# Kernel optimization log

Hardware: AMD Instinct MI355X
Metric: run time of the kernel (lower is better)

Reference implementation:

```python
import jax, jax.numpy as jnp
import numpy as np

B, T, D, U = 128, 1024, 256, 256


def setup_inputs() -> dict:
    key = jax.random.key(0)
    ks = jax.random.split(key, 16)
    s_in = 1.0 / np.sqrt(D)
    s_rec = 1.0 / np.sqrt(U)
    inp = {"x": jax.random.normal(ks[0], (B, T, D), dtype=jnp.float32)}
    for i, name in enumerate(["wf", "wi", "wc", "wo"]):
        inp[name] = jax.random.normal(ks[1 + i], (D, U), dtype=jnp.float32) * s_in
    for i, name in enumerate(["rf", "ri", "rc", "ro", "pf", "pi", "po"]):
        inp[name] = jax.random.normal(ks[5 + i], (U, U), dtype=jnp.float32) * s_rec
    for i, name in enumerate(["bf", "bi", "bc", "bo"]):
        inp[name] = jax.random.normal(ks[12 + i], (U,), dtype=jnp.float32) * 0.01
    return inp


def reference(x, wf, wi, wc, wo, rf, ri, rc, ro, pf, pi, po, bf, bi, bc, bo):
    # Peephole LSTM: scan over time, state (c, h) each [B, U].
    def step(carry, xt):
        c, h = carry
        f_gate = jax.nn.sigmoid(xt @ wf + h @ rf + c @ pf + bf)
        i_gate = jax.nn.sigmoid(xt @ wi + h @ ri + c @ pi + bi)
        c_tild = jnp.tanh(xt @ wc + h @ rc + bc)
        c_new = f_gate * c + i_gate * c_tild
        o_gate = jax.nn.sigmoid(xt @ wo + h @ ro + c_new @ po + bo)
        h_new = jnp.tanh(c_new) * o_gate
        return (c_new, h_new), None

    b = x.shape[0]
    u = wf.shape[1]
    c0 = jnp.zeros((b, u), dtype=x.dtype)
    h0 = jnp.zeros((b, u), dtype=x.dtype)
    (_, h_final), _ = jax.lax.scan(step, (c0, h0), jnp.swapaxes(x, 0, 1))  # time-major [T,B,D]
    return h_final
```

## Files before the change

### kernel.cpp

```cpp
#include <hip/hip_runtime.h>

#define TT 1024
#define DU 256

#define CEX_OFF   0
#define HEX_OFF   65536
#define STMP_OFF  131072
#define TST_OFF   139264
#define GCON_OFF  172032
#define BLOB_OFF  174080
#define CHUNK_ELEMS (11*16*256)

typedef unsigned short ushort_t;
typedef unsigned u32;
typedef unsigned long long u64;
typedef __attribute__((ext_vector_type(8))) short short8;
typedef __attribute__((ext_vector_type(2))) unsigned long long u64x2;
typedef __attribute__((ext_vector_type(4))) float floatx4;

#define MFMA(a, b, c) __builtin_amdgcn_mfma_f32_16x16x32_bf16((a), (b), (c), 0, 0, 0)

__device__ __forceinline__ ushort_t f2bf(float f) {
  unsigned u = __float_as_uint(f);
  return (ushort_t)((u + 0x7fffu + ((u >> 16) & 1u)) >> 16);
}
__device__ __forceinline__ float sigf(float x) { return 1.0f / (1.0f + __expf(-x)); }
__device__ __forceinline__ float tanhf_(float x) {
  float t = 1.0f - 2.0f / (__expf(2.0f * fabsf(x)) + 1.0f);
  return copysignf(t, x);
}

__device__ __forceinline__ short8 ldfrag(const ushort_t* p) {
  union { struct { u64 a, b; } q; short8 s; } v;
  v.q.a = __hip_atomic_load((const u64*)p,       __ATOMIC_RELAXED, __HIP_MEMORY_SCOPE_AGENT);
  v.q.b = __hip_atomic_load((const u64*)(p + 4), __ATOMIC_RELAXED, __HIP_MEMORY_SCOPE_AGENT);
  return v.s;
}
__device__ __forceinline__ void wait_slow(const u32* stG, u32 tgt, int lane) {
  const u32* p = stG + (lane & 15) * 16 + ((lane >> 4) & 1);
  for (;;) {
    u32 s = __hip_atomic_load(p, __ATOMIC_RELAXED, __HIP_MEMORY_SCOPE_AGENT);
    if (__all((int)(s >= tgt))) return;
    __builtin_amdgcn_s_sleep(1);
  }
}

__device__ __forceinline__ u32 poll_nt(const u32* p) {
  u32 s;
  asm volatile("global_load_dword %0, %1, off nt\n\ts_waitcnt vmcnt(0)"
               : "=v"(s) : "v"(p) : "memory");
  return s;
}
__device__ __forceinline__ int wait_fast(const u32* stG, u32 tgt, int lane) {
  const u32* p = stG + (lane & 15) * 16 + ((lane >> 4) & 1);
  int it = 0;
  for (;;) {
    u32 s = poll_nt(p);
    if (__all((int)(s >= tgt))) return 1;
    if (++it > 16384) return 0;
  }
}
__device__ __forceinline__ short8 ldfrag_nt(const ushort_t* p) {
  union { u64x2 q; short8 s; } v;
  v.q = __builtin_nontemporal_load((const u64x2*)p);
  return v.s;
}

__device__ int test_nt(u32* tb, int mem, int lane) {
  u64* td = (u64*)tb;
  u32* tstamp = tb + 256;
  u32* tready = tb + 512;
  int ok = 1;
  for (int r = 0; r < 3; ++r) {
    u32 seq = 1u + (u32)r;
    if (lane == 0)
      __hip_atomic_store(tready + mem, seq, __ATOMIC_RELEASE, __HIP_MEMORY_SCOPE_AGENT);
    { int it = 0;
      for (;;) {
        u32 v = __hip_atomic_load(tready + (lane & 15), __ATOMIC_RELAXED,
                                  __HIP_MEMORY_SCOPE_AGENT);
        if (__all((int)(v >= seq))) break;
        if (++it > 16384) return 0;
        __builtin_amdgcn_s_sleep(2);
      } }
    if (lane < 8) {
      u64 v = 0x9E3779B97F4A7C15ull * (u64)(seq * 131u + (u32)mem * 17u + (u32)lane + 1u);
      asm volatile("global_store_dwordx2 %0, %1, off"
                   :: "v"(td + mem * 8 + lane), "v"(v) : "memory");
    }
    asm volatile("s_waitcnt vmcnt(0)" ::: "memory");
    if (lane == 0)
      asm volatile("global_store_dword %0, %1, off"
                   :: "v"(tstamp + mem * 16), "v"(seq) : "memory");
    int saw = 0;
    { int it = 0;
      for (;;) {
        u32 s = poll_nt(tstamp + (lane & 15) * 16);
        if (__all((int)(s >= seq))) { saw = 1; break; }
        if (++it > 192) break;
        __builtin_amdgcn_s_sleep(2);
      } }
    if (!saw) { ok = 0; continue; }
    u64 a = __builtin_nontemporal_load(td + lane);
    u64 b = __builtin_nontemporal_load(td + lane + 64);
    int s0 = lane >> 3, j0 = lane & 7, s1 = (lane + 64) >> 3, j1 = (lane + 64) & 7;
    u64 e0 = 0x9E3779B97F4A7C15ull * (u64)(seq * 131u + (u32)s0 * 17u + (u32)j0 + 1u);
    u64 e1 = 0x9E3779B97F4A7C15ull * (u64)(seq * 131u + (u32)s1 * 17u + (u32)j1 + 1u);
    if (!__all((int)((a == e0) && (b == e1)))) ok = 0;
  }
  return ok;
}

__global__ void conv_weights(
    const float* __restrict__ wf, const float* __restrict__ wi,
    const float* __restrict__ wc, const float* __restrict__ wo,
    const float* __restrict__ rf, const float* __restrict__ ri,
    const float* __restrict__ rc, const float* __restrict__ ro,
    const float* __restrict__ pf, const float* __restrict__ pi,
    const float* __restrict__ po, ushort_t* __restrict__ blob)
{
  int id = blockIdx.x * 256 + threadIdx.x;
  int k   = id & 255;
  int col = (id >> 8) & 15;
  int q   = id >> 12;
  int m   = q % 11;
  int mm  = q / 11;
  const float* srcs[11] = {wf, wi, wc, wo, rf, ri, rc, ro, pf, pi, po};
  float v = srcs[m][k * 256 + mm * 16 + col];
  unsigned u = __float_as_uint(v);
  blob[id] = (ushort_t)((u + 0x7fffu + ((u >> 16) & 1u)) >> 16);
}

extern "C" __global__ void __launch_bounds__(128, 1)
lstm_rec(const float* __restrict__ x, const ushort_t* __restrict__ blob,
         ushort_t* __restrict__ h_ex, ushort_t* __restrict__ c_ex,
         u32* __restrict__ stamps, u32* __restrict__ tst, u32* __restrict__ gcon,
         const float* __restrict__ bfv, const float* __restrict__ biv,
         const float* __restrict__ bcv, const float* __restrict__ bov,
         float* __restrict__ out)
{
  __shared__ ushort_t xa[16 * 264];
  __shared__ float pre[4][16][17];
  __shared__ float pop[16][17];
  __shared__ float bia[4][16];
  __shared__ int s_mode;

  const int tid = threadIdx.x;
  const int bid = blockIdx.x;
  const int wv = tid >> 6;
  const int lane = tid & 63;
  const int lr = lane & 15;
  const int lk = lane >> 4;

  const int grp = bid & 7;
  const int mem = bid >> 3;
  const int gb0 = grp * 16;
  const int gc0 = mem * 16;

  u32* gok  = gcon;
  u32* gpol = gcon + 256;

  if (wv == 0) {
    __builtin_amdgcn_fence(__ATOMIC_ACQUIRE, "agent");
    int okv = test_nt(tst + grp * 1024, mem, lane);
    if (lane == 0)
      __hip_atomic_store(gok + bid, 1u | ((u32)okv << 1),
                         __ATOMIC_RELEASE, __HIP_MEMORY_SCOPE_AGENT);
    if (bid == 0) {
      u32 pol = 0; int it = 0;
      for (;;) {
        u32 a = __hip_atomic_load(gok + lane, __ATOMIC_RELAXED, __HIP_MEMORY_SCOPE_AGENT);
        u32 b = __hip_atomic_load(gok + 64 + lane, __ATOMIC_RELAXED, __HIP_MEMORY_SCOPE_AGENT);
        if (__all((int)((a & 1u) && (b & 1u)))) {
          pol = __all((int)(((a >> 1) & 1u) && ((b >> 1) & 1u))) ? 1u : 0u;
          break;
        }
        if (++it > 32768) { pol = 0; break; }
        __builtin_amdgcn_s_sleep(4);
      }
      if (lane == 0)
        __hip_atomic_store(gpol, pol + 1u, __ATOMIC_RELEASE, __HIP_MEMORY_SCOPE_AGENT);
    }
    u32 p;
    for (;;) {
      p = __hip_atomic_load(gpol, __ATOMIC_RELAXED, __HIP_MEMORY_SCOPE_AGENT);
      if (p) break;
      __builtin_amdgcn_s_sleep(4);
    }
    if (lane == 0) s_mode = (int)(p - 1u);
  }
  __syncthreads();
  const int fast = s_mode;
  int wedged = 0;
  if (fast) __builtin_amdgcn_fence(__ATOMIC_ACQUIRE, "agent");

  const ushort_t* wb = blob + (size_t)mem * CHUNK_ELEMS;
  short8 wXa[8], wXb[8], wRa[8], wRb[8], wPa[8], wPb[8];
  {
    const int m0 = wv ? 2 : 0;
    const int p0 = wv ? 10 : 8;
    const int p1 = wv ? 10 : 9;
#pragma unroll
    for (int s = 0; s < 8; ++s) {
      const int ko = s * 32 + lk * 8;
      wXa[s] = *(const short8*)(wb + ((m0    ) * 16 + lr) * 256 + ko);
      wXb[s] = *(const short8*)(wb + ((m0 + 1) * 16 + lr) * 256 + ko);
      wRa[s] = *(const short8*)(wb + ((m0 + 4) * 16 + lr) * 256 + ko);
      wRb[s] = *(const short8*)(wb + ((m0 + 5) * 16 + lr) * 256 + ko);
      wPa[s] = *(const short8*)(wb + (p0 * 16 + lr) * 256 + ko);
      wPb[s] = *(const short8*)(wb + (p1 * 16 + lr) * 256 + ko);
    }
  }

  if (tid < 64) {
    const float* bs = (tid < 16) ? bfv : (tid < 32) ? biv : (tid < 48) ? bcv : bov;
    bia[tid >> 4][tid & 15] = bs[gc0 + (tid & 15)];
  }
  const int pb = tid >> 3, pc = (tid & 7) * 2;
  float cr0 = 0.f, cr1 = 0.f;

  const int xr = tid >> 3, xc = (tid & 7) * 32;
  {
    const float* xp = x + (size_t)(gb0 + xr) * TT * DU + xc;
#pragma unroll
    for (int u = 0; u < 8; ++u) {
      float4 f = *(const float4*)(xp + u * 4);
      *(u64*)&xa[xr * 264 + xc + u * 4] =
          (u64)f2bf(f.x) | ((u64)f2bf(f.y) << 16) |
          ((u64)f2bf(f.z) << 32) | ((u64)f2bf(f.w) << 48);
    }
  }
  __syncthreads();

  const floatx4 z4 = {0.f, 0.f, 0.f, 0.f};
  floatx4 accA = z4, accB = z4;
#pragma unroll
  for (int s = 0; s < 8; ++s) {
    short8 a = *(const short8*)&xa[lr * 264 + s * 32 + lk * 8];
    accA = MFMA(a, wXa[s], accA);
    accB = MFMA(a, wXb[s], accB);
  }

  u32* stG = stamps + grp * 256;
  ushort_t* cG = c_ex + grp * 16 * 256;
  ushort_t* hG = h_ex + grp * 16 * 256;
  u32* cSlot = (u32*)(cG + mem * 256 + pb * 16 + pc);
  u32* hSlot = (u32*)(hG + mem * 256 + pb * 16 + pc);
  u32* mySt  = stG + mem * 16 + wv;

  for (int t = 0; t < TT; ++t) {
    if (t > 0) {
      if (fast) { if (!wedged && !wait_fast(stG, 2u * (u32)t, lane)) wedged = 1; }
      else wait_slow(stG, 2u * (u32)t, lane);
      short8 hf[8];
#pragma unroll
      for (int s = 0; s < 8; ++s) {
        int k = s * 32 + lk * 8;
        hf[s] = fast ? ldfrag_nt(hG + (k >> 4) * 256 + lr * 16 + (k & 15))
                     : ldfrag(hG + (k >> 4) * 256 + lr * 16 + (k & 15));
      }
#pragma unroll
      for (int s = 0; s < 8; ++s) {
        accA = MFMA(hf[s], wRa[s], accA);
        accB = MFMA(hf[s], wRb[s], accB);
      }
    }
#pragma unroll
    for (int r = 0; r < 4; ++r) {
      pre[wv * 2    ][lk * 4 + r][lr] = accA[r];
      pre[wv * 2 + 1][lk * 4 + r][lr] = accB[r];
    }
    __syncthreads();

    {
      float fg = sigf(pre[0][pb][pc] + bia[0][pc]);
      float ig = sigf(pre[1][pb][pc] + bia[1][pc]);
      float ct = tanhf_(pre[2][pb][pc] + bia[2][pc]);
      cr0 = fg * cr0 + ig * ct;
      fg = sigf(pre[0][pb][pc + 1] + bia[0][pc + 1]);
      ig = sigf(pre[1][pb][pc + 1] + bia[1][pc + 1]);
      ct = tanhf_(pre[2][pb][pc + 1] + bia[2][pc + 1]);
      cr1 = fg * cr1 + ig * ct;
    }
    {
      u32 cw = (u32)f2bf(cr0) | ((u32)f2bf(cr1) << 16);
      if (fast)
        asm volatile("global_store_dword %0, %1, off" :: "v"(cSlot), "v"(cw) : "memory");
      else
        __hip_atomic_store(cSlot, cw, __ATOMIC_RELAXED, __HIP_MEMORY_SCOPE_AGENT);
      asm volatile("s_waitcnt vmcnt(0)" ::: "memory");
      if (lane == 0) {
        u32 sv = 2u * (u32)t + 1u;
        if (fast)
          asm volatile("global_store_dword %0, %1, off" :: "v"(mySt), "v"(sv) : "memory");
        else
          __hip_atomic_store(mySt, sv, __ATOMIC_RELAXED, __HIP_MEMORY_SCOPE_AGENT);
      }
    }

    if (t < TT - 1) {
      float4 xf[8];
      const float* xp = x + ((size_t)(gb0 + xr) * TT + (t + 1)) * DU + xc;
#pragma unroll
      for (int u = 0; u < 8; ++u) xf[u] = *(const float4*)(xp + u * 4);
#pragma unroll
      for (int u = 0; u < 8; ++u) {
        float4 f = xf[u];
        *(u64*)&xa[xr * 264 + xc + u * 4] =
            (u64)f2bf(f.x) | ((u64)f2bf(f.y) << 16) |
            ((u64)f2bf(f.z) << 32) | ((u64)f2bf(f.w) << 48);
      }
      __syncthreads();
    }

    if (fast) { if (!wedged && !wait_fast(stG, 2u * (u32)t + 1u, lane)) wedged = 1; }
    else wait_slow(stG, 2u * (u32)t + 1u, lane);

    {
      short8 cf[8];
#pragma unroll
      for (int s = 0; s < 8; ++s) {
        int k = s * 32 + lk * 8;
        cf[s] = fast ? ldfrag_nt(cG + (k >> 4) * 256 + lr * 16 + (k & 15))
                     : ldfrag(cG + (k >> 4) * 256 + lr * 16 + (k & 15));
      }
      if (wv == 0) {
        accA = z4; accB = z4;
#pragma unroll
        for (int s = 0; s < 8; ++s) {
          accA = MFMA(cf[s], wPa[s], accA);
          accB = MFMA(cf[s], wPb[s], accB);
        }
      } else {
        floatx4 pacc = z4;
#pragma unroll
        for (int s = 0; s < 8; ++s)
          pacc = MFMA(cf[s], wPa[s], pacc);
#pragma unroll
        for (int r = 0; r < 4; ++r) pop[lk * 4 + r][lr] = pacc[r];
      }
    }
    __syncthreads();

    float og0 = sigf(pre[3][pb][pc] + pop[pb][pc] + bia[3][pc]);
    float hv0 = tanhf_(cr0) * og0;
    float og1 = sigf(pre[3][pb][pc + 1] + pop[pb][pc + 1] + bia[3][pc + 1]);
    float hv1 = tanhf_(cr1) * og1;
    if (t == TT - 1) {
      float2 o2; o2.x = hv0; o2.y = hv1;
      *(float2*)&out[(gb0 + pb) * 256 + gc0 + pc] = o2;
      break;
    }
    {
      u32 hw = (u32)f2bf(hv0) | ((u32)f2bf(hv1) << 16);
      if (fast)
        asm volatile("global_store_dword %0, %1, off" :: "v"(hSlot), "v"(hw) : "memory");
      else
        __hip_atomic_store(hSlot, hw, __ATOMIC_RELAXED, __HIP_MEMORY_SCOPE_AGENT);
      asm volatile("s_waitcnt vmcnt(0)" ::: "memory");
      if (lane == 0) {
        u32 sv = 2u * (u32)t + 2u;
        if (fast)
          asm volatile("global_store_dword %0, %1, off" :: "v"(mySt), "v"(sv) : "memory");
        else
          __hip_atomic_store(mySt, sv, __ATOMIC_RELAXED, __HIP_MEMORY_SCOPE_AGENT);
      }
    }

    if (wv == 1) { accA = z4; accB = z4; }
#pragma unroll
    for (int s = 0; s < 8; ++s) {
      short8 a = *(const short8*)&xa[lr * 264 + s * 32 + lk * 8];
      accA = MFMA(a, wXa[s], accA);
      accB = MFMA(a, wXb[s], accB);
    }
  }
}

extern "C" void kernel_launch(void* const* d_in, const int* in_sizes, int n_in,
                              void* d_out, int out_size, void* d_ws, size_t ws_size,
                              hipStream_t stream) {
  const float* x   = (const float*)d_in[0];
  const float* bfv = (const float*)d_in[12];
  const float* biv = (const float*)d_in[13];
  const float* bcv = (const float*)d_in[14];
  const float* bov = (const float*)d_in[15];
  float* outp = (float*)d_out;

  char* ws = (char*)d_ws;
  ushort_t* c_exp = (ushort_t*)(ws + CEX_OFF);
  ushort_t* h_exp = (ushort_t*)(ws + HEX_OFF);
  u32* stmp = (u32*)(ws + STMP_OFF);
  u32* tstp = (u32*)(ws + TST_OFF);
  u32* gcon = (u32*)(ws + GCON_OFF);
  ushort_t* blob = (ushort_t*)(ws + BLOB_OFF);

  hipMemsetAsync(d_ws, 0, BLOB_OFF, stream);

  hipLaunchKernelGGL(conv_weights, dim3(2816), dim3(256), 0, stream,
                     (const float*)d_in[1], (const float*)d_in[2],
                     (const float*)d_in[3], (const float*)d_in[4],
                     (const float*)d_in[5], (const float*)d_in[6],
                     (const float*)d_in[7], (const float*)d_in[8],
                     (const float*)d_in[9], (const float*)d_in[10],
                     (const float*)d_in[11], blob);

  hipLaunchKernelGGL(lstm_rec, dim3(128), dim3(128), 0, stream,
                     x, (const ushort_t*)blob, h_exp, c_exp, stmp, tstp, gcon,
                     bfv, biv, bcv, bov, outp);
}
```

Baseline: 3.338 ms.

## Add sc0 cross-block polling mode and pack per-group stamps contiguously

Adds a third synchronisation mode that uses sc0-cached global loads for stamp polling and for fetching the exchanged h/c fragments. A startup self-test runs for both nt and sc0 modes and picks sc0 when every block passes. The per-group stamp array is packed from a 16-stride layout into 32 contiguous words, so a wave's poll touches fewer cache lines. The fragment loads are issued as a batch followed by one wait, which cuts latency on the per-timestep critical path. The risk is that sc0 visibility across CUs may not hold on every run, and the longer self-test adds startup cost.

```diff
diff --git a/kernel.cpp b/kernel.cpp
--- a/kernel.cpp
+++ b/kernel.cpp
@@ -37,7 +37,7 @@
   return v.s;
 }
 __device__ __forceinline__ void wait_slow(const u32* stG, u32 tgt, int lane) {
-  const u32* p = stG + (lane & 15) * 16 + ((lane >> 4) & 1);
+  const u32* p = stG + (lane & 31);
   for (;;) {
     u32 s = __hip_atomic_load(p, __ATOMIC_RELAXED, __HIP_MEMORY_SCOPE_AGENT);
     if (__all((int)(s >= tgt))) return;
@@ -45,17 +45,21 @@
   }
 }
 
-__device__ __forceinline__ u32 poll_nt(const u32* p) {
+__device__ __forceinline__ u32 poll_f(const u32* p, int mode) {
   u32 s;
-  asm volatile("global_load_dword %0, %1, off nt\n\ts_waitcnt vmcnt(0)"
-               : "=v"(s) : "v"(p) : "memory");
+  if (mode == 2)
+    asm volatile("global_load_dword %0, %1, off sc0\n\ts_waitcnt vmcnt(0)"
+                 : "=v"(s) : "v"(p) : "memory");
+  else
+    asm volatile("global_load_dword %0, %1, off nt\n\ts_waitcnt vmcnt(0)"
+                 : "=v"(s) : "v"(p) : "memory");
   return s;
 }
-__device__ __forceinline__ int wait_fast(const u32* stG, u32 tgt, int lane) {
-  const u32* p = stG + (lane & 15) * 16 + ((lane >> 4) & 1);
+__device__ __forceinline__ int wait_f(const u32* stG, u32 tgt, int lane, int mode) {
+  const u32* p = stG + (lane & 31);
   int it = 0;
   for (;;) {
-    u32 s = poll_nt(p);
+    u32 s = poll_f(p, mode);
     if (__all((int)(s >= tgt))) return 1;
     if (++it > 16384) return 0;
   }
@@ -65,8 +69,13 @@
   v.q = __builtin_nontemporal_load((const u64x2*)p);
   return v.s;
 }
-
-__device__ int test_nt(u32* tb, int mem, int lane) {
+__device__ __forceinline__ short8 ldfrag_sc0_issue(const ushort_t* p) {
+  short8 v;
+  asm volatile("global_load_dwordx4 %0, %1, off sc0" : "=v"(v) : "v"(p));
+  return v;
+}
+
+__device__ int test_pipe(u32* tb, int mem, int lane, int mode) {
   u64* td = (u64*)tb;
   u32* tstamp = tb + 256;
   u32* tready = tb + 512;
@@ -95,14 +104,22 @@
     int saw = 0;
     { int it = 0;
       for (;;) {
-        u32 s = poll_nt(tstamp + (lane & 15) * 16);
+        u32 s = poll_f(tstamp + (lane & 15) * 16, mode);
         if (__all((int)(s >= seq))) { saw = 1; break; }
         if (++it > 192) break;
         __builtin_amdgcn_s_sleep(2);
       } }
     if (!saw) { ok = 0; continue; }
-    u64 a = __builtin_nontemporal_load(td + lane);
-    u64 b = __builtin_nontemporal_load(td + lane + 64);
+    u64 a, b;
+    if (mode == 2) {
+      asm volatile("global_load_dwordx2 %0, %2, off sc0\n\t"
+                   "global_load_dwordx2 %1, %3, off sc0\n\t"
+                   "s_waitcnt vmcnt(0)"
+                   : "=v"(a), "=v"(b) : "v"(td + lane), "v"(td + lane + 64) : "memory");
+    } else {
+      a = __builtin_nontemporal_load(td + lane);
+      b = __builtin_nontemporal_load(td + lane + 64);
+    }
     int s0 = lane >> 3, j0 = lane & 7, s1 = (lane + 64) >> 3, j1 = (lane + 64) & 7;
     u64 e0 = 0x9E3779B97F4A7C15ull * (u64)(seq * 131u + (u32)s0 * 17u + (u32)j0 + 1u);
     u64 e1 = 0x9E3779B97F4A7C15ull * (u64)(seq * 131u + (u32)s1 * 17u + (u32)j1 + 1u);
@@ -162,9 +179,10 @@
 
   if (wv == 0) {
     __builtin_amdgcn_fence(__ATOMIC_ACQUIRE, "agent");
-    int okv = test_nt(tst + grp * 1024, mem, lane);
+    int okNT = test_pipe(tst + 0 * 2048 + grp * 256, mem, lane, 1);
+    int okS0 = test_pipe(tst + 1 * 2048 + grp * 256, mem, lane, 2);
     if (lane == 0)
-      __hip_atomic_store(gok + bid, 1u | ((u32)okv << 1),
+      __hip_atomic_store(gok + bid, 1u | ((u32)okNT << 1) | ((u32)okS0 << 2),
                          __ATOMIC_RELEASE, __HIP_MEMORY_SCOPE_AGENT);
     if (bid == 0) {
       u32 pol = 0; int it = 0;
@@ -172,7 +190,8 @@
         u32 a = __hip_atomic_load(gok + lane, __ATOMIC_RELAXED, __HIP_MEMORY_SCOPE_AGENT);
         u32 b = __hip_atomic_load(gok + 64 + lane, __ATOMIC_RELAXED, __HIP_MEMORY_SCOPE_AGENT);
         if (__all((int)((a & 1u) && (b & 1u)))) {
-          pol = __all((int)(((a >> 1) & 1u) && ((b >> 1) & 1u))) ? 1u : 0u;
+          if      (__all((int)(((a >> 2) & 1u) && ((b >> 2) & 1u)))) pol = 2;
+          else if (__all((int)(((a >> 1) & 1u) && ((b >> 1) & 1u)))) pol = 1;
           break;
         }
         if (++it > 32768) { pol = 0; break; }
@@ -190,9 +209,9 @@
     if (lane == 0) s_mode = (int)(p - 1u);
   }
   __syncthreads();
-  const int fast = s_mode;
+  const int mode = s_mode;
   int wedged = 0;
-  if (fast) __builtin_amdgcn_fence(__ATOMIC_ACQUIRE, "agent");
+  if (mode) __builtin_amdgcn_fence(__ATOMIC_ACQUIRE, "agent");
 
   const ushort_t* wb = blob + (size_t)mem * CHUNK_ELEMS;
   short8 wXa[8], wXb[8], wRa[8], wRb[8], wPa[8], wPb[8];
@@ -241,23 +260,33 @@
     accB = MFMA(a, wXb[s], accB);
   }
 
-  u32* stG = stamps + grp * 256;
+  u32* stG = stamps + grp * 32;
   ushort_t* cG = c_ex + grp * 16 * 256;
   ushort_t* hG = h_ex + grp * 16 * 256;
   u32* cSlot = (u32*)(cG + mem * 256 + pb * 16 + pc);
   u32* hSlot = (u32*)(hG + mem * 256 + pb * 16 + pc);
-  u32* mySt  = stG + mem * 16 + wv;
+  u32* mySt  = stG + mem * 2 + wv;
 
   for (int t = 0; t < TT; ++t) {
     if (t > 0) {
-      if (fast) { if (!wedged && !wait_fast(stG, 2u * (u32)t, lane)) wedged = 1; }
+      if (mode) { if (!wedged && !wait_f(stG, 2u * (u32)t, lane, mode)) wedged = 1; }
       else wait_slow(stG, 2u * (u32)t, lane);
       short8 hf[8];
-#pragma unroll
-      for (int s = 0; s < 8; ++s) {
-        int k = s * 32 + lk * 8;
-        hf[s] = fast ? ldfrag_nt(hG + (k >> 4) * 256 + lr * 16 + (k & 15))
-                     : ldfrag(hG + (k >> 4) * 256 + lr * 16 + (k & 15));
+      if (mode == 2) {
+#pragma unroll
+        for (int s = 0; s < 8; ++s) {
+          int k = s * 32 + lk * 8;
+          hf[s] = ldfrag_sc0_issue(hG + (k >> 4) * 256 + lr * 16 + (k & 15));
+        }
+        asm volatile("s_waitcnt vmcnt(0)" ::: "memory");
+        __builtin_amdgcn_sched_barrier(0);
+      } else {
+#pragma unroll
+        for (int s = 0; s < 8; ++s) {
+          int k = s * 32 + lk * 8;
+          hf[s] = mode ? ldfrag_nt(hG + (k >> 4) * 256 + lr * 16 + (k & 15))
+                       : ldfrag(hG + (k >> 4) * 256 + lr * 16 + (k & 15));
+        }
       }
 #pragma unroll
       for (int s = 0; s < 8; ++s) {
@@ -284,14 +313,14 @@
     }
     {
       u32 cw = (u32)f2bf(cr0) | ((u32)f2bf(cr1) << 16);
-      if (fast)
+      if (mode)
         asm volatile("global_store_dword %0, %1, off" :: "v"(cSlot), "v"(cw) : "memory");
       else
         __hip_atomic_store(cSlot, cw, __ATOMIC_RELAXED, __HIP_MEMORY_SCOPE_AGENT);
       asm volatile("s_waitcnt vmcnt(0)" ::: "memory");
       if (lane == 0) {
         u32 sv = 2u * (u32)t + 1u;
-        if (fast)
+        if (mode)
           asm volatile("global_store_dword %0, %1, off" :: "v"(mySt), "v"(sv) : "memory");
         else
           __hip_atomic_store(mySt, sv, __ATOMIC_RELAXED, __HIP_MEMORY_SCOPE_AGENT);
@@ -313,16 +342,26 @@
       __syncthreads();
     }
 
-    if (fast) { if (!wedged && !wait_fast(stG, 2u * (u32)t + 1u, lane)) wedged = 1; }
+    if (mode) { if (!wedged && !wait_f(stG, 2u * (u32)t + 1u, lane, mode)) wedged = 1; }
     else wait_slow(stG, 2u * (u32)t + 1u, lane);
 
     {
       short8 cf[8];
-#pragma unroll
-      for (int s = 0; s < 8; ++s) {
-        int k = s * 32 + lk * 8;
-        cf[s] = fast ? ldfrag_nt(cG + (k >> 4) * 256 + lr * 16 + (k & 15))
-                     : ldfrag(cG + (k >> 4) * 256 + lr * 16 + (k & 15));
+      if (mode == 2) {
+#pragma unroll
+        for (int s = 0; s < 8; ++s) {
+          int k = s * 32 + lk * 8;
+          cf[s] = ldfrag_sc0_issue(cG + (k >> 4) * 256 + lr * 16 + (k & 15));
+        }
+        asm volatile("s_waitcnt vmcnt(0)" ::: "memory");
+        __builtin_amdgcn_sched_barrier(0);
+      } else {
+#pragma unroll
+        for (int s = 0; s < 8; ++s) {
+          int k = s * 32 + lk * 8;
+          cf[s] = mode ? ldfrag_nt(cG + (k >> 4) * 256 + lr * 16 + (k & 15))
+                       : ldfrag(cG + (k >> 4) * 256 + lr * 16 + (k & 15));
+        }
       }
       if (wv == 0) {
         accA = z4; accB = z4;
@@ -353,14 +392,14 @@
     }
     {
       u32 hw = (u32)f2bf(hv0) | ((u32)f2bf(hv1) << 16);
-      if (fast)
+      if (mode)
         asm volatile("global_store_dword %0, %1, off" :: "v"(hSlot), "v"(hw) : "memory");
       else
         __hip_atomic_store(hSlot, hw, __ATOMIC_RELAXED, __HIP_MEMORY_SCOPE_AGENT);
       asm volatile("s_waitcnt vmcnt(0)" ::: "memory");
       if (lane == 0) {
         u32 sv = 2u * (u32)t + 2u;
-        if (fast)
+        if (mode)
           asm volatile("global_store_dword %0, %1, off" :: "v"(mySt), "v"(sv) : "memory");
         else
           __hip_atomic_store(mySt, sv, __ATOMIC_RELAXED, __HIP_MEMORY_SCOPE_AGENT);
```

Measured after the change: 3.816 ms. 14.3% more time.

## Split LSTM gate matmuls along K across waves and wait on half the producers

Applied to the files above, without the earlier changes.

Each of the two waves previously owned two full gates across the whole 256-wide K dimension. Now each wave computes all four gates over its own half of K, and the partial sums are added through shared memory. Each wave polls only the stamps of the producer blocks whose h/c columns it actually reads, and the stamp array is packed densely. This shortens the serial MFMA chain per wave and the fan-in of each wait, and the f/i peephole product is folded into the next step's accumulator. The cost is extra shared-memory reductions, and the denser stamps may cause more polling contention on shared cache lines.

```diff
diff --git a/kernel.cpp b/kernel.cpp
--- a/kernel.cpp
+++ b/kernel.cpp
@@ -36,8 +36,8 @@
   v.q.b = __hip_atomic_load((const u64*)(p + 4), __ATOMIC_RELAXED, __HIP_MEMORY_SCOPE_AGENT);
   return v.s;
 }
-__device__ __forceinline__ void wait_slow(const u32* stG, u32 tgt, int lane) {
-  const u32* p = stG + (lane & 15) * 16 + ((lane >> 4) & 1);
+__device__ __forceinline__ void wait_half_slow(const u32* stG, u32 tgt, int lane, int wv) {
+  const u32* p = stG + (wv * 8 + (lane & 7)) * 2 + ((lane >> 3) & 1);
   for (;;) {
     u32 s = __hip_atomic_load(p, __ATOMIC_RELAXED, __HIP_MEMORY_SCOPE_AGENT);
     if (__all((int)(s >= tgt))) return;
@@ -51,8 +51,8 @@
                : "=v"(s) : "v"(p) : "memory");
   return s;
 }
-__device__ __forceinline__ int wait_fast(const u32* stG, u32 tgt, int lane) {
-  const u32* p = stG + (lane & 15) * 16 + ((lane >> 4) & 1);
+__device__ __forceinline__ int wait_half_f(const u32* stG, u32 tgt, int lane, int wv) {
+  const u32* p = stG + (wv * 8 + (lane & 7)) * 2 + ((lane >> 3) & 1);
   int it = 0;
   for (;;) {
     u32 s = poll_nt(p);
@@ -140,8 +140,8 @@
          float* __restrict__ out)
 {
   __shared__ ushort_t xa[16 * 264];
-  __shared__ float pre[4][16][17];
-  __shared__ float pop[16][17];
+  __shared__ float pre2[2][4][16][17];
+  __shared__ float pop2[2][16][17];
   __shared__ float bia[4][16];
   __shared__ int s_mode;
 
@@ -190,26 +190,23 @@
     if (lane == 0) s_mode = (int)(p - 1u);
   }
   __syncthreads();
-  const int fast = s_mode;
+  const int mode = s_mode;
   int wedged = 0;
-  if (fast) __builtin_amdgcn_fence(__ATOMIC_ACQUIRE, "agent");
+  if (mode) __builtin_amdgcn_fence(__ATOMIC_ACQUIRE, "agent");
 
   const ushort_t* wb = blob + (size_t)mem * CHUNK_ELEMS;
-  short8 wXa[8], wXb[8], wRa[8], wRb[8], wPa[8], wPb[8];
-  {
-    const int m0 = wv ? 2 : 0;
-    const int p0 = wv ? 10 : 8;
-    const int p1 = wv ? 10 : 9;
-#pragma unroll
-    for (int s = 0; s < 8; ++s) {
-      const int ko = s * 32 + lk * 8;
-      wXa[s] = *(const short8*)(wb + ((m0    ) * 16 + lr) * 256 + ko);
-      wXb[s] = *(const short8*)(wb + ((m0 + 1) * 16 + lr) * 256 + ko);
-      wRa[s] = *(const short8*)(wb + ((m0 + 4) * 16 + lr) * 256 + ko);
-      wRb[s] = *(const short8*)(wb + ((m0 + 5) * 16 + lr) * 256 + ko);
-      wPa[s] = *(const short8*)(wb + (p0 * 16 + lr) * 256 + ko);
-      wPb[s] = *(const short8*)(wb + (p1 * 16 + lr) * 256 + ko);
-    }
+  short8 wW[4][4], wR[4][4], wPf[4], wPi[4], wPo[4];
+#pragma unroll
+  for (int s = 0; s < 4; ++s) {
+    const int ko = wv * 128 + s * 32 + lk * 8;
+#pragma unroll
+    for (int g = 0; g < 4; ++g) {
+      wW[g][s] = *(const short8*)(wb + ((g    ) * 16 + lr) * 256 + ko);
+      wR[g][s] = *(const short8*)(wb + ((4 + g) * 16 + lr) * 256 + ko);
+    }
+    wPf[s] = *(const short8*)(wb + (8  * 16 + lr) * 256 + ko);
+    wPi[s] = *(const short8*)(wb + (9  * 16 + lr) * 256 + ko);
+    wPo[s] = *(const short8*)(wb + (10 * 16 + lr) * 256 + ko);
   }
 
   if (tid < 64) {
@@ -233,65 +230,70 @@
   __syncthreads();
 
   const floatx4 z4 = {0.f, 0.f, 0.f, 0.f};
-  floatx4 accA = z4, accB = z4;
-#pragma unroll
-  for (int s = 0; s < 8; ++s) {
-    short8 a = *(const short8*)&xa[lr * 264 + s * 32 + lk * 8];
-    accA = MFMA(a, wXa[s], accA);
-    accB = MFMA(a, wXb[s], accB);
-  }
-
-  u32* stG = stamps + grp * 256;
+  floatx4 acc[4] = {z4, z4, z4, z4};
+#pragma unroll
+  for (int s = 0; s < 4; ++s) {
+    int k = wv * 128 + s * 32 + lk * 8;
+    short8 a = *(const short8*)&xa[lr * 264 + k];
+    acc[0] = MFMA(a, wW[0][s], acc[0]);
+    acc[1] = MFMA(a, wW[1][s], acc[1]);
+    acc[2] = MFMA(a, wW[2][s], acc[2]);
+    acc[3] = MFMA(a, wW[3][s], acc[3]);
+  }
+
+  u32* stG = stamps + grp * 32;
   ushort_t* cG = c_ex + grp * 16 * 256;
   ushort_t* hG = h_ex + grp * 16 * 256;
   u32* cSlot = (u32*)(cG + mem * 256 + pb * 16 + pc);
   u32* hSlot = (u32*)(hG + mem * 256 + pb * 16 + pc);
-  u32* mySt  = stG + mem * 16 + wv;
+  u32* mySt  = stG + mem * 2 + wv;
 
   for (int t = 0; t < TT; ++t) {
     if (t > 0) {
-      if (fast) { if (!wedged && !wait_fast(stG, 2u * (u32)t, lane)) wedged = 1; }
-      else wait_slow(stG, 2u * (u32)t, lane);
-      short8 hf[8];
-#pragma unroll
-      for (int s = 0; s < 8; ++s) {
-        int k = s * 32 + lk * 8;
-        hf[s] = fast ? ldfrag_nt(hG + (k >> 4) * 256 + lr * 16 + (k & 15))
+      if (mode) { if (!wedged && !wait_half_f(stG, 2u * (u32)t, lane, wv)) wedged = 1; }
+      else wait_half_slow(stG, 2u * (u32)t, lane, wv);
+      short8 hf[4];
+#pragma unroll
+      for (int s = 0; s < 4; ++s) {
+        int k = wv * 128 + s * 32 + lk * 8;
+        hf[s] = mode ? ldfrag_nt(hG + (k >> 4) * 256 + lr * 16 + (k & 15))
                      : ldfrag(hG + (k >> 4) * 256 + lr * 16 + (k & 15));
       }
 #pragma unroll
-      for (int s = 0; s < 8; ++s) {
-        accA = MFMA(hf[s], wRa[s], accA);
-        accB = MFMA(hf[s], wRb[s], accB);
-      }
-    }
-#pragma unroll
-    for (int r = 0; r < 4; ++r) {
-      pre[wv * 2    ][lk * 4 + r][lr] = accA[r];
-      pre[wv * 2 + 1][lk * 4 + r][lr] = accB[r];
-    }
+      for (int s = 0; s < 4; ++s) {
+        acc[0] = MFMA(hf[s], wR[0][s], acc[0]);
+        acc[1] = MFMA(hf[s], wR[1][s], acc[1]);
+        acc[2] = MFMA(hf[s], wR[2][s], acc[2]);
+        acc[3] = MFMA(hf[s], wR[3][s], acc[3]);
+      }
+    }
+#pragma unroll
+    for (int g = 0; g < 4; ++g)
+#pragma unroll
+      for (int r = 0; r < 4; ++r)
+        pre2[wv][g][lk * 4 + r][lr] = acc[g][r];
     __syncthreads();
 
     {
-      float fg = sigf(pre[0][pb][pc] + bia[0][pc]);
-      float ig = sigf(pre[1][pb][pc] + bia[1][pc]);
-      float ct = tanhf_(pre[2][pb][pc] + bia[2][pc]);
+      float fg = sigf(pre2[0][0][pb][pc] + pre2[1][0][pb][pc] + bia[0][pc]);
+      float ig = sigf(pre2[0][1][pb][pc] + pre2[1][1][pb][pc] + bia[1][pc]);
+      float ct = tanhf_(pre2[0][2][pb][pc] + pre2[1][2][pb][pc] + bia[2][pc]);
       cr0 = fg * cr0 + ig * ct;
-      fg = sigf(pre[0][pb][pc + 1] + bia[0][pc + 1]);
-      ig = sigf(pre[1][pb][pc + 1] + bia[1][pc + 1]);
-      ct = tanhf_(pre[2][pb][pc + 1] + bia[2][pc + 1]);
+      fg = sigf(pre2[0][0][pb][pc + 1] + pre2[1][0][pb][pc + 1] + bia[0][pc + 1]);
+      ig = sigf(pre2[0][1][pb][pc + 1] + pre2[1][1][pb][pc + 1] + bia[1][pc + 1]);
+      ct = tanhf_(pre2[0][2][pb][pc + 1] + pre2[1][2][pb][pc + 1] + bia[2][pc + 1]);
       cr1 = fg * cr1 + ig * ct;
     }
     {
       u32 cw = (u32)f2bf(cr0) | ((u32)f2bf(cr1) << 16);
-      if (fast)
+      if (mode)
         asm volatile("global_store_dword %0, %1, off" :: "v"(cSlot), "v"(cw) : "memory");
       else
         __hip_atomic_store(cSlot, cw, __ATOMIC_RELAXED, __HIP_MEMORY_SCOPE_AGENT);
       asm volatile("s_waitcnt vmcnt(0)" ::: "memory");
       if (lane == 0) {
         u32 sv = 2u * (u32)t + 1u;
-        if (fast)
+        if (mode)
           asm volatile("global_store_dword %0, %1, off" :: "v"(mySt), "v"(sv) : "memory");
         else
           __hip_atomic_store(mySt, sv, __ATOMIC_RELAXED, __HIP_MEMORY_SCOPE_AGENT);
@@ -313,38 +315,30 @@
       __syncthreads();
     }
 
-    if (fast) { if (!wedged && !wait_fast(stG, 2u * (u32)t + 1u, lane)) wedged = 1; }
-    else wait_slow(stG, 2u * (u32)t + 1u, lane);
-
+    if (mode) { if (!wedged && !wait_half_f(stG, 2u * (u32)t + 1u, lane, wv)) wedged = 1; }
+    else wait_half_slow(stG, 2u * (u32)t + 1u, lane, wv);
+
+    short8 cf[4];
+#pragma unroll
+    for (int s = 0; s < 4; ++s) {
+      int k = wv * 128 + s * 32 + lk * 8;
+      cf[s] = mode ? ldfrag_nt(cG + (k >> 4) * 256 + lr * 16 + (k & 15))
+                   : ldfrag(cG + (k >> 4) * 256 + lr * 16 + (k & 15));
+    }
     {
-      short8 cf[8];
-#pragma unroll
-      for (int s = 0; s < 8; ++s) {
-        int k = s * 32 + lk * 8;
-        cf[s] = fast ? ldfrag_nt(cG + (k >> 4) * 256 + lr * 16 + (k & 15))
-                     : ldfrag(cG + (k >> 4) * 256 + lr * 16 + (k & 15));
-      }
-      if (wv == 0) {
-        accA = z4; accB = z4;
-#pragma unroll
-        for (int s = 0; s < 8; ++s) {
-          accA = MFMA(cf[s], wPa[s], accA);
-          accB = MFMA(cf[s], wPb[s], accB);
-        }
-      } else {
-        floatx4 pacc = z4;
-#pragma unroll
-        for (int s = 0; s < 8; ++s)
-          pacc = MFMA(cf[s], wPa[s], pacc);
-#pragma unroll
-        for (int r = 0; r < 4; ++r) pop[lk * 4 + r][lr] = pacc[r];
-      }
+      floatx4 pacc = z4;
+#pragma unroll
+      for (int s = 0; s < 4; ++s) pacc = MFMA(cf[s], wPo[s], pacc);
+#pragma unroll
+      for (int r = 0; r < 4; ++r) pop2[wv][lk * 4 + r][lr] = pacc[r];
     }
     __syncthreads();
 
-    float og0 = sigf(pre[3][pb][pc] + pop[pb][pc] + bia[3][pc]);
+    float og0 = sigf(pre2[0][3][pb][pc] + pre2[1][3][pb][pc]
+                   + pop2[0][pb][pc] + pop2[1][pb][pc] + bia[3][pc]);
     float hv0 = tanhf_(cr0) * og0;
-    float og1 = sigf(pre[3][pb][pc + 1] + pop[pb][pc + 1] + bia[3][pc + 1]);
+    float og1 = sigf(pre2[0][3][pb][pc + 1] + pre2[1][3][pb][pc + 1]
+                   + pop2[0][pb][pc + 1] + pop2[1][pb][pc + 1] + bia[3][pc + 1]);
     float hv1 = tanhf_(cr1) * og1;
     if (t == TT - 1) {
       float2 o2; o2.x = hv0; o2.y = hv1;
@@ -353,26 +347,35 @@
     }
     {
       u32 hw = (u32)f2bf(hv0) | ((u32)f2bf(hv1) << 16);
-      if (fast)
+      if (mode)
         asm volatile("global_store_dword %0, %1, off" :: "v"(hSlot), "v"(hw) : "memory");
       else
         __hip_atomic_store(hSlot, hw, __ATOMIC_RELAXED, __HIP_MEMORY_SCOPE_AGENT);
       asm volatile("s_waitcnt vmcnt(0)" ::: "memory");
       if (lane == 0) {
         u32 sv = 2u * (u32)t + 2u;
-        if (fast)
+        if (mode)
           asm volatile("global_store_dword %0, %1, off" :: "v"(mySt), "v"(sv) : "memory");
         else
           __hip_atomic_store(mySt, sv, __ATOMIC_RELAXED, __HIP_MEMORY_SCOPE_AGENT);
       }
     }
 
-    if (wv == 1) { accA = z4; accB = z4; }
-#pragma unroll
-    for (int s = 0; s < 8; ++s) {
-      short8 a = *(const short8*)&xa[lr * 264 + s * 32 + lk * 8];
-      accA = MFMA(a, wXa[s], accA);
-      accB = MFMA(a, wXb[s], accB);
+#pragma unroll
+    for (int g = 0; g < 4; ++g) acc[g] = z4;
+#pragma unroll
+    for (int s = 0; s < 4; ++s) {
+      int k = wv * 128 + s * 32 + lk * 8;
+      short8 a = *(const short8*)&xa[lr * 264 + k];
+      acc[0] = MFMA(a, wW[0][s], acc[0]);
+      acc[1] = MFMA(a, wW[1][s], acc[1]);
+      acc[2] = MFMA(a, wW[2][s], acc[2]);
+      acc[3] = MFMA(a, wW[3][s], acc[3]);
+    }
+#pragma unroll
+    for (int s = 0; s < 4; ++s) {
+      acc[0] = MFMA(cf[s], wPf[s], acc[0]);
+      acc[1] = MFMA(cf[s], wPi[s], acc[1]);
     }
   }
 }
```

Result: faster. 3.001 ms (-10.1%).
